# Kernel tuning notes

Hardware: AMD Instinct MI355X
Metric: run time of the kernel (lower is better)

The kernel has to match this reference:

```python
import jax, jax.numpy as jnp
import numpy as np

ALPHA = 0.5  # smooth_quant migration strength
N_TOKENS, D_MODEL = 32768, 1024  # square linear: d_in == d_out (required by diag_s @ weight)


def setup_inputs() -> dict:
    key = jax.random.key(0)
    k1, k2, k3 = jax.random.split(key, 3)
    x = jax.random.normal(k1, (N_TOKENS, D_MODEL), dtype=jnp.float32)
    weight = jax.random.normal(k2, (D_MODEL, D_MODEL), dtype=jnp.float32) * 0.02
    bias = jax.random.normal(k3, (D_MODEL,), dtype=jnp.float32) * 0.02
    return {"x": x, "weight": weight, "bias": bias}


def reference(x, weight, bias):
    # SmoothQuant rescale: per-in-channel maxima of activations and weight.
    max_act = jnp.max(x, axis=0) ** ALPHA                 # [D]
    max_w = jnp.max(weight, axis=0) ** (1.0 - ALPHA)      # [D] (max over out dim -> per in-channel)
    s = max_act / max_w                                   # [D] scale_fact
    # x_hat = x @ diag(s)^-1 ; expressed as the equivalent per-channel broadcast.
    x_hat = x / s                                         # [N, D]
    # weight_hat = diag(s) @ weight (square linear, row rescale).
    w_hat = s[:, None] * weight                           # [D, D]
    # nn.Linear forward: x_hat @ weight_hat^T + bias
    return x_hat @ w_hat.T + bias
```

## Files before the change

### kernel.cpp

```cpp
#include <hip/hip_runtime.h>
#include <hip/hip_bf16.h>
#include <stdint.h>

#define D_MODEL 1024

typedef __attribute__((ext_vector_type(4))) float  f32x4;
typedef __attribute__((ext_vector_type(8))) __bf16 bf16x8;
typedef __attribute__((ext_vector_type(8))) unsigned short u16x8;
typedef __attribute__((ext_vector_type(4))) unsigned short u16x4;


__device__ __forceinline__ unsigned order_map(float x) {
    unsigned u = __float_as_uint(x);
    return (u & 0x80000000u) ? ~u : (u | 0x80000000u);
}
__device__ __forceinline__ float order_unmap(unsigned m) {
    unsigned b = (m & 0x80000000u) ? (m & 0x7fffffffu) : ~m;
    return __uint_as_float(b);
}
__device__ __forceinline__ unsigned short f2bf(float f) {
    unsigned u = __float_as_uint(f);
    u += 0x7fffu + ((u >> 16) & 1u);
    return (unsigned short)(u >> 16);
}


__global__ void init_u32(unsigned* __restrict__ p, int n) {
    int i = blockIdx.x * blockDim.x + threadIdx.x;
    if (i < n) p[i] = 0u;
}

__global__ void colmax_kernel(const float* __restrict__ src, int rows_per_slab,
                              int cols, unsigned* __restrict__ out_u) {
    int k = blockIdx.x * blockDim.x + threadIdx.x;
    const float* p = src + (size_t)blockIdx.y * rows_per_slab * cols + k;
    float m = -__builtin_inff();
#pragma unroll 4
    for (int r = 0; r < rows_per_slab; ++r)
        m = fmaxf(m, p[(size_t)r * cols]);
    atomicMax(&out_u[k], order_map(m));
}

#define CC_ROWS 16
__global__ __launch_bounds__(256)
void colmax_convert(const float* __restrict__ x,
                    float* __restrict__ partial,
                    unsigned short* __restrict__ xb) {
    int c4 = threadIdx.x * 4;
    size_t base = (size_t)blockIdx.x * CC_ROWS * D_MODEL + c4;
    f32x4 m4 = {-__builtin_inff(), -__builtin_inff(), -__builtin_inff(), -__builtin_inff()};
#pragma unroll 8
    for (int r = 0; r < CC_ROWS; ++r) {
        f32x4 v = *reinterpret_cast<const f32x4*>(&x[base + (size_t)r * D_MODEL]);
        u16x4 o;
#pragma unroll
        for (int e = 0; e < 4; ++e) { m4[e] = fmaxf(m4[e], v[e]); o[e] = f2bf(v[e]); }
        *reinterpret_cast<u16x4*>(&xb[base + (size_t)r * D_MODEL]) = o;
    }
    *reinterpret_cast<f32x4*>(&partial[(size_t)blockIdx.x * D_MODEL + c4]) = m4;
}

__global__ void reduce_partial(const float* __restrict__ partial,
                               unsigned* __restrict__ ma_u) {
    int col  = blockIdx.x * 256 + threadIdx.x;
    int b0   = blockIdx.y * 64;
    float m = -__builtin_inff();
#pragma unroll 8
    for (int i = 0; i < 64; ++i)
        m = fmaxf(m, partial[(size_t)(b0 + i) * D_MODEL + col]);
    atomicMax(&ma_u[col], order_map(m));
}

__global__ void scale_kernel(const unsigned* __restrict__ ma_u,
                             const unsigned* __restrict__ mw_u,
                             float* __restrict__ s) {
    int k = blockIdx.x * blockDim.x + threadIdx.x;
    if (k < D_MODEL) {
        float ma = order_unmap(ma_u[k]);
        float mw = order_unmap(mw_u[k]);
        s[k] = sqrtf(ma) / sqrtf(mw);
    }
}

__global__ void build_w_kernel(const float* __restrict__ W, const float* __restrict__ s,
                               unsigned short* __restrict__ Wp) {
    int j  = blockIdx.x;
    int k4 = threadIdx.x * 4;
    float sj = s[j];
    f32x4 w  = *reinterpret_cast<const f32x4*>(&W[(size_t)j * D_MODEL + k4]);
    f32x4 sk = *reinterpret_cast<const f32x4*>(&s[k4]);
    u16x4 o;
#pragma unroll
    for (int i = 0; i < 4; ++i) o[i] = f2bf(sj * w[i] / sk[i]);
    *reinterpret_cast<u16x4*>(&Wp[(size_t)j * D_MODEL + k4]) = o;
}

#define GBM 256
#define GBN 256
#define GBK 64
#define GNT (D_MODEL / GBK)

__global__ __launch_bounds__(512, 2)
void gemm_8ph(const unsigned short* __restrict__ Xb,
              const unsigned short* __restrict__ Wp,
              const float* __restrict__ bias,
              float* __restrict__ out) {
    __shared__ __align__(16) unsigned short As[2][GBM][GBK];
    __shared__ __align__(16) unsigned short Bs[2][GBN][GBK];

    int flat = blockIdx.x;
    int swz  = (flat & 7) * (gridDim.x >> 3) + (flat >> 3);
    const int nRowBlk = 32768 / GBM;
    int row0 = (swz % nRowBlk) * GBM;
    int col0 = (swz / nRowBlk) * GBN;

    int tid  = threadIdx.x;
    int wave = tid >> 6;
    int lane = tid & 63;
    int wr   = wave >> 2;
    int wc   = wave & 3;
    int l16  = lane & 15;
    int lq   = lane >> 4;
    int srow  = lane >> 3;
    int skoff = ((lane & 7) ^ srow) << 3;

    f32x4 acc[2][2][4][2];
#pragma unroll
    for (int mq = 0; mq < 2; ++mq)
#pragma unroll
        for (int nq = 0; nq < 2; ++nq)
#pragma unroll
            for (int m = 0; m < 4; ++m)
#pragma unroll
                for (int n = 0; n < 2; ++n)
                    acc[mq][nq][m][n] = (f32x4){0.f, 0.f, 0.f, 0.f};

    auto stageA = [&](int t, int b) {
        int k0 = t * GBK;
#pragma unroll
        for (int i = 0; i < 4; ++i) {
            int rg = wave * 4 + i;
            const unsigned short* g = Xb + (size_t)(row0 + rg * 8 + srow) * D_MODEL + k0 + skoff;
            __builtin_amdgcn_global_load_lds(
                (const __attribute__((address_space(1))) void*)g,
                (__attribute__((address_space(3))) void*)&As[b][rg * 8][0], 16, 0, 0);
        }
    };
    auto stageB = [&](int t, int b) {
        int k0 = t * GBK;
#pragma unroll
        for (int i = 0; i < 4; ++i) {
            int rg = wave * 4 + i;
            const unsigned short* g = Wp + (size_t)(col0 + rg * 8 + srow) * D_MODEL + k0 + skoff;
            __builtin_amdgcn_global_load_lds(
                (const __attribute__((address_space(1))) void*)g,
                (__attribute__((address_space(3))) void*)&Bs[b][rg * 8][0], 16, 0, 0);
        }
    };

    stageA(0, 0); stageB(0, 0);
    asm volatile("s_waitcnt vmcnt(0)" ::: "memory");
    __builtin_amdgcn_s_barrier();

#pragma unroll 1
    for (int t = 0; t < GNT; ++t) {
        int cur = t & 1;
        const char* Ab = (const char*)&As[cur][0][0];
        const char* Bb = (const char*)&Bs[cur][0][0];
        bool pf = (t < GNT - 1);

        bf16x8 af[4][2], bf[2][2];

        auto lda = [&](int mq, int m, int kk) {
            int row  = wr * 128 + mq * 64 + m * 16 + l16;
            int slot = (kk * 4 + lq) ^ (row & 7);
            return *reinterpret_cast<const bf16x8*>(Ab + row * 128 + slot * 16);
        };
        auto ldb = [&](int nq, int n, int kk) {
            int row  = wc * 64 + nq * 32 + n * 16 + l16;
            int slot = (kk * 4 + lq) ^ (row & 7);
            return *reinterpret_cast<const bf16x8*>(Bb + row * 128 + slot * 16);
        };
        auto quad = [&](int mq, int nq) {
            __builtin_amdgcn_s_setprio(1);
#pragma unroll
            for (int m = 0; m < 4; ++m)
#pragma unroll
                for (int n = 0; n < 2; ++n)
#pragma unroll
                    for (int kk = 0; kk < 2; ++kk)
                        acc[mq][nq][m][n] = __builtin_amdgcn_mfma_f32_16x16x32_bf16(
                            af[m][kk], bf[n][kk], acc[mq][nq][m][n], 0, 0, 0);
            __builtin_amdgcn_s_setprio(0);
        };

#pragma unroll
        for (int m = 0; m < 4; ++m)
#pragma unroll
            for (int kk = 0; kk < 2; ++kk) af[m][kk] = lda(0, m, kk);
#pragma unroll
        for (int n = 0; n < 2; ++n)
#pragma unroll
            for (int kk = 0; kk < 2; ++kk) bf[n][kk] = ldb(0, n, kk);
        if (pf) stageA(t + 1, cur ^ 1);
        __builtin_amdgcn_s_barrier();
        quad(0, 0);
        __builtin_amdgcn_s_barrier();

#pragma unroll
        for (int n = 0; n < 2; ++n)
#pragma unroll
            for (int kk = 0; kk < 2; ++kk) bf[n][kk] = ldb(1, n, kk);
        if (pf) stageB(t + 1, cur ^ 1);
        __builtin_amdgcn_s_barrier();
        quad(0, 1);
        __builtin_amdgcn_s_barrier();

#pragma unroll
        for (int m = 0; m < 4; ++m)
#pragma unroll
            for (int kk = 0; kk < 2; ++kk) af[m][kk] = lda(1, m, kk);
        __builtin_amdgcn_s_barrier();
        quad(1, 1);
        __builtin_amdgcn_s_barrier();

#pragma unroll
        for (int n = 0; n < 2; ++n)
#pragma unroll
            for (int kk = 0; kk < 2; ++kk) bf[n][kk] = ldb(0, n, kk);
        __builtin_amdgcn_s_barrier();
        quad(1, 0);
        if (pf) {
            asm volatile("s_waitcnt vmcnt(0)" ::: "memory");
            __builtin_amdgcn_s_barrier();
        }
    }

    int crow = row0 + wr * 128;
    int ccol = col0 + wc * 64;
#pragma unroll
    for (int nq = 0; nq < 2; ++nq)
#pragma unroll
        for (int n = 0; n < 2; ++n) {
            int col = ccol + nq * 32 + n * 16 + l16;
            float b = bias[col];
#pragma unroll
            for (int mq = 0; mq < 2; ++mq)
#pragma unroll
                for (int m = 0; m < 4; ++m) {
                    int r = crow + mq * 64 + m * 16 + lq * 4;
#pragma unroll
                    for (int q = 0; q < 4; ++q)
                        out[(size_t)(r + q) * D_MODEL + col] = acc[mq][nq][m][n][q] + b;
                }
        }
}

__global__ __launch_bounds__(256)
void gemm_fallback(const float* __restrict__ X, const unsigned short* __restrict__ Wp,
                   const float* __restrict__ bias, float* __restrict__ out, int N) {
    __shared__ __align__(16) unsigned short As[128][64];
    __shared__ __align__(16) unsigned short Bs[128][64];

    int flat = blockIdx.x;
    int swz  = ((gridDim.x & 7) == 0)
             ? (flat & 7) * (gridDim.x >> 3) + (flat >> 3) : flat;
    const int nColBlk = D_MODEL / 128;
    int row0 = (swz / nColBlk) * 128;
    int col0 = (swz % nColBlk) * 128;

    int tid  = threadIdx.x;
    int wave = tid >> 6;
    int lane = tid & 63;
    int wr   = wave >> 1;
    int wc   = wave & 1;
    int l16  = lane & 15;
    int srow  = lane >> 3;
    int skoff = ((lane & 7) ^ srow) << 3;

    f32x4 acc[4][4];
#pragma unroll
    for (int m = 0; m < 4; ++m)
#pragma unroll
        for (int n = 0; n < 4; ++n)
            acc[m][n] = (f32x4){0.f, 0.f, 0.f, 0.f};

    for (int k0 = 0; k0 < D_MODEL; k0 += 64) {
        __syncthreads();
#pragma unroll
        for (int i = 0; i < 4; ++i) {
            int c   = i * 256 + tid;
            int r   = c >> 3;
            int seg = c & 7;
            const float* gp = X + (size_t)(row0 + r) * D_MODEL + k0 + seg * 8;
            f32x4 x0 = *reinterpret_cast<const f32x4*>(gp);
            f32x4 x1 = *reinterpret_cast<const f32x4*>(gp + 4);
            u16x8 v;
#pragma unroll
            for (int e = 0; e < 4; ++e) { v[e] = f2bf(x0[e]); v[e + 4] = f2bf(x1[e]); }
            int off = (seg * 16) ^ ((r & 7) << 4);
            *reinterpret_cast<u16x8*>((char*)&As[0][0] + r * 128 + off) = v;
        }
#pragma unroll
        for (int i = 0; i < 4; ++i) {
            int r0 = (wave * 4 + i) * 8;
            const unsigned short* g = Wp + (size_t)(col0 + r0 + srow) * D_MODEL + k0 + skoff;
            __builtin_amdgcn_global_load_lds(
                (const __attribute__((address_space(1))) void*)g,
                (__attribute__((address_space(3))) void*)&Bs[r0][0], 16, 0, 0);
        }
        __syncthreads();
#pragma unroll
        for (int kk = 0; kk < 2; ++kk) {
            bf16x8 af[4], bf_[4];
#pragma unroll
            for (int m = 0; m < 4; ++m) {
                int row = wr * 64 + m * 16 + l16;
                int o   = ((lane >> 4) * 16 + kk * 64) ^ ((row & 7) << 4);
                af[m] = *reinterpret_cast<const bf16x8*>((const char*)&As[0][0] + row * 128 + o);
            }
#pragma unroll
            for (int n = 0; n < 4; ++n) {
                int row = wc * 64 + n * 16 + l16;
                int o   = ((lane >> 4) * 16 + kk * 64) ^ ((row & 7) << 4);
                bf_[n] = *reinterpret_cast<const bf16x8*>((const char*)&Bs[0][0] + row * 128 + o);
            }
#pragma unroll
            for (int m = 0; m < 4; ++m)
#pragma unroll
                for (int n = 0; n < 4; ++n)
                    acc[m][n] = __builtin_amdgcn_mfma_f32_16x16x32_bf16(
                        af[m], bf_[n], acc[m][n], 0, 0, 0);
        }
    }

    int crow = row0 + wr * 64;
    int ccol = col0 + wc * 64;
#pragma unroll
    for (int n = 0; n < 4; ++n) {
        int col = ccol + n * 16 + l16;
        float b = bias[col];
#pragma unroll
        for (int m = 0; m < 4; ++m) {
            int r = crow + m * 16 + (lane >> 4) * 4;
#pragma unroll
            for (int q = 0; q < 4; ++q)
                out[(size_t)(r + q) * D_MODEL + col] = acc[m][n][q] + b;
        }
    }
}


extern "C" void kernel_launch(void* const* d_in, const int* in_sizes, int n_in,
                              void* d_out, int out_size, void* d_ws, size_t ws_size,
                              hipStream_t stream) {
    const float* x    = (const float*)d_in[0];
    const float* w    = (const float*)d_in[1];
    const float* bias = (const float*)d_in[2];
    float* out        = (float*)d_out;
    const int N       = in_sizes[0] / D_MODEL;

    char* ws               = (char*)d_ws;
    unsigned*       ma_u   = (unsigned*)(ws);
    unsigned*       mw_u   = (unsigned*)(ws + 4096);
    float*          s      = (float*)(ws + 8192);
    unsigned short* Wp     = (unsigned short*)(ws + 16384);
    unsigned short* Xb     = (unsigned short*)(ws + 16384 + (size_t)D_MODEL * D_MODEL * 2);
    const int nPart        = N / CC_ROWS;
    float*          part   = (float*)(ws + 16384 + (size_t)D_MODEL * D_MODEL * 2
                                               + (size_t)N * D_MODEL * 2);

    size_t need = 16384 + (size_t)D_MODEL * D_MODEL * 2 + (size_t)N * D_MODEL * 2
                + (size_t)nPart * D_MODEL * 4;
    bool preconv = ws_size >= need;

    init_u32<<<8, 256, 0, stream>>>((unsigned*)ws, 2048);

    if (preconv) {
        colmax_convert<<<nPart, 256, 0, stream>>>(x, part, Xb);
        reduce_partial<<<dim3(D_MODEL / 256, nPart / 64), 256, 0, stream>>>(part, ma_u);
    } else {
        colmax_kernel<<<dim3(D_MODEL / 256, 64), 256, 0, stream>>>(x, N / 64, D_MODEL, ma_u);
    }
    colmax_kernel<<<dim3(D_MODEL / 256, 16), 256, 0, stream>>>(w, D_MODEL / 16, D_MODEL, mw_u);
    scale_kernel<<<D_MODEL / 256, 256, 0, stream>>>(ma_u, mw_u, s);
    build_w_kernel<<<D_MODEL, 256, 0, stream>>>(w, s, Wp);

    if (preconv) {
        int nblk = (N / GBM) * (D_MODEL / GBN);
        gemm_8ph<<<nblk, 512, 0, stream>>>(Xb, Wp, bias, out);
    } else {
        int nblk = (N / 128) * (D_MODEL / 128);
        gemm_fallback<<<nblk, 256, 0, stream>>>(x, Wp, bias, out, N);
    }
}
```

Baseline: 170.8 us.

## Replace 8-phase barrier schedule with upfront prefetch and XCD-aware tile mapping

The main GEMM loop drops the four barrier-separated quadrant phases. It now issues the next tile's global-to-LDS loads at the top of each iteration, loads all B fragments once, and runs two half-tile MFMA blocks with a single barrier per k-step. Block-to-tile mapping changes so that each XCD gets a fixed column block and a contiguous range of row blocks, which is meant to improve L2 reuse of the weight tile. Fewer barriers should cut stalls, but holding more B fragments raises register pressure. Issuing all prefetch loads at once also changes how memory latency overlaps with compute.

```diff
diff --git a/kernel.cpp b/kernel.cpp
--- a/kernel.cpp
+++ b/kernel.cpp
@@ -101,18 +101,18 @@
 #define GNT (D_MODEL / GBK)
 
 __global__ __launch_bounds__(512, 2)
-void gemm_8ph(const unsigned short* __restrict__ Xb,
-              const unsigned short* __restrict__ Wp,
-              const float* __restrict__ bias,
-              float* __restrict__ out) {
+void gemm_main(const unsigned short* __restrict__ Xb,
+               const unsigned short* __restrict__ Wp,
+               const float* __restrict__ bias,
+               float* __restrict__ out) {
     __shared__ __align__(16) unsigned short As[2][GBM][GBK];
     __shared__ __align__(16) unsigned short Bs[2][GBN][GBK];
 
     int flat = blockIdx.x;
-    int swz  = (flat & 7) * (gridDim.x >> 3) + (flat >> 3);
-    const int nRowBlk = 32768 / GBM;
-    int row0 = (swz % nRowBlk) * GBM;
-    int col0 = (swz / nRowBlk) * GBN;
+    int xcd  = flat & 7;
+    int idx  = flat >> 3;
+    int col0 = (xcd & 3) * GBN;
+    int row0 = ((xcd >> 2) * 64 + idx) * GBM;
 
     int tid  = threadIdx.x;
     int wave = tid >> 6;
@@ -165,11 +165,11 @@
 #pragma unroll 1
     for (int t = 0; t < GNT; ++t) {
         int cur = t & 1;
+        bool pf = (t + 1 < GNT);
         const char* Ab = (const char*)&As[cur][0][0];
         const char* Bb = (const char*)&Bs[cur][0][0];
-        bool pf = (t < GNT - 1);
-
-        bf16x8 af[4][2], bf[2][2];
+
+        if (pf) { stageA(t + 1, cur ^ 1); stageB(t + 1, cur ^ 1); }
 
         auto lda = [&](int mq, int m, int kk) {
             int row  = wr * 128 + mq * 64 + m * 16 + l16;
@@ -181,55 +181,55 @@
             int slot = (kk * 4 + lq) ^ (row & 7);
             return *reinterpret_cast<const bf16x8*>(Bb + row * 128 + slot * 16);
         };
-        auto quad = [&](int mq, int nq) {
+
+        bf16x8 bf[2][2][2];
+#pragma unroll
+        for (int nq = 0; nq < 2; ++nq)
+#pragma unroll
+            for (int n = 0; n < 2; ++n)
+#pragma unroll
+                for (int kk = 0; kk < 2; ++kk)
+                    bf[nq][n][kk] = ldb(nq, n, kk);
+
+        {
+            bf16x8 af[4][2];
+#pragma unroll
+            for (int m = 0; m < 4; ++m)
+#pragma unroll
+                for (int kk = 0; kk < 2; ++kk) af[m][kk] = lda(0, m, kk);
             __builtin_amdgcn_s_setprio(1);
 #pragma unroll
             for (int m = 0; m < 4; ++m)
 #pragma unroll
-                for (int n = 0; n < 2; ++n)
-#pragma unroll
-                    for (int kk = 0; kk < 2; ++kk)
-                        acc[mq][nq][m][n] = __builtin_amdgcn_mfma_f32_16x16x32_bf16(
-                            af[m][kk], bf[n][kk], acc[mq][nq][m][n], 0, 0, 0);
+                for (int nq = 0; nq < 2; ++nq)
+#pragma unroll
+                    for (int n = 0; n < 2; ++n)
+#pragma unroll
+                        for (int kk = 0; kk < 2; ++kk)
+                            acc[0][nq][m][n] = __builtin_amdgcn_mfma_f32_16x16x32_bf16(
+                                af[m][kk], bf[nq][n][kk], acc[0][nq][m][n], 0, 0, 0);
             __builtin_amdgcn_s_setprio(0);
-        };
-
-#pragma unroll
-        for (int m = 0; m < 4; ++m)
-#pragma unroll
-            for (int kk = 0; kk < 2; ++kk) af[m][kk] = lda(0, m, kk);
-#pragma unroll
-        for (int n = 0; n < 2; ++n)
-#pragma unroll
-            for (int kk = 0; kk < 2; ++kk) bf[n][kk] = ldb(0, n, kk);
-        if (pf) stageA(t + 1, cur ^ 1);
-        __builtin_amdgcn_s_barrier();
-        quad(0, 0);
-        __builtin_amdgcn_s_barrier();
-
-#pragma unroll
-        for (int n = 0; n < 2; ++n)
-#pragma unroll
-            for (int kk = 0; kk < 2; ++kk) bf[n][kk] = ldb(1, n, kk);
-        if (pf) stageB(t + 1, cur ^ 1);
-        __builtin_amdgcn_s_barrier();
-        quad(0, 1);
-        __builtin_amdgcn_s_barrier();
-
-#pragma unroll
-        for (int m = 0; m < 4; ++m)
-#pragma unroll
-            for (int kk = 0; kk < 2; ++kk) af[m][kk] = lda(1, m, kk);
-        __builtin_amdgcn_s_barrier();
-        quad(1, 1);
-        __builtin_amdgcn_s_barrier();
-
-#pragma unroll
-        for (int n = 0; n < 2; ++n)
-#pragma unroll
-            for (int kk = 0; kk < 2; ++kk) bf[n][kk] = ldb(0, n, kk);
-        __builtin_amdgcn_s_barrier();
-        quad(1, 0);
+        }
+        {
+            bf16x8 af[4][2];
+#pragma unroll
+            for (int m = 0; m < 4; ++m)
+#pragma unroll
+                for (int kk = 0; kk < 2; ++kk) af[m][kk] = lda(1, m, kk);
+            __builtin_amdgcn_s_setprio(1);
+#pragma unroll
+            for (int m = 0; m < 4; ++m)
+#pragma unroll
+                for (int nq = 0; nq < 2; ++nq)
+#pragma unroll
+                    for (int n = 0; n < 2; ++n)
+#pragma unroll
+                        for (int kk = 0; kk < 2; ++kk)
+                            acc[1][nq][m][n] = __builtin_amdgcn_mfma_f32_16x16x32_bf16(
+                                af[m][kk], bf[nq][n][kk], acc[1][nq][m][n], 0, 0, 0);
+            __builtin_amdgcn_s_setprio(0);
+        }
+
         if (pf) {
             asm volatile("s_waitcnt vmcnt(0)" ::: "memory");
             __builtin_amdgcn_s_barrier();
@@ -388,7 +388,7 @@
 
     if (preconv) {
         int nblk = (N / GBM) * (D_MODEL / GBN);
-        gemm_8ph<<<nblk, 512, 0, stream>>>(Xb, Wp, bias, out);
+        gemm_main<<<nblk, 512, 0, stream>>>(Xb, Wp, bias, out);
     } else {
         int nblk = (N / 128) * (D_MODEL / 128);
         gemm_fallback<<<nblk, 256, 0, stream>>>(x, Wp, bias, out, N);
```

After: 168.0 us. About the same (-1.7%).

## Split GEMM tile prefetch into four chunks with partial vmcnt waits and XCD-aware mapping

Applied to the files above, without the earlier changes.

The next K-tile prefetch is split into four chunks, one issued in each compute phase. Each phase waits with a partial s_waitcnt vmcnt(4) instead of a full drain at the end of the iteration, so global-to-LDS loads overlap the MFMA work more evenly. The block-to-tile mapping now places consecutive row blocks and all four column blocks on the same XCD to improve L2 reuse. The launch-bounds occupancy hint of 2 is dropped. The partial-wait counting must exactly match the number of outstanding loads, or a phase could read an LDS chunk before it has fully landed.

```diff
diff --git a/kernel.cpp b/kernel.cpp
--- a/kernel.cpp
+++ b/kernel.cpp
@@ -100,19 +100,19 @@
 #define GBK 64
 #define GNT (D_MODEL / GBK)
 
-__global__ __launch_bounds__(512, 2)
-void gemm_8ph(const unsigned short* __restrict__ Xb,
-              const unsigned short* __restrict__ Wp,
-              const float* __restrict__ bias,
-              float* __restrict__ out) {
+__global__ __launch_bounds__(512)
+void gemm_main(const unsigned short* __restrict__ Xb,
+               const unsigned short* __restrict__ Wp,
+               const float* __restrict__ bias,
+               float* __restrict__ out) {
     __shared__ __align__(16) unsigned short As[2][GBM][GBK];
     __shared__ __align__(16) unsigned short Bs[2][GBN][GBK];
 
-    int flat = blockIdx.x;
-    int swz  = (flat & 7) * (gridDim.x >> 3) + (flat >> 3);
-    const int nRowBlk = 32768 / GBM;
-    int row0 = (swz % nRowBlk) * GBM;
-    int col0 = (swz / nRowBlk) * GBN;
+    int flat  = blockIdx.x;
+    int xcd   = flat & 7;
+    int j     = flat >> 3;
+    int col0  = (j & 3) * GBN;
+    int row0  = ((xcd << 4) + (j >> 2)) * GBM;
 
     int tid  = threadIdx.x;
     int wave = tid >> 6;
@@ -135,51 +135,53 @@
                 for (int n = 0; n < 2; ++n)
                     acc[mq][nq][m][n] = (f32x4){0.f, 0.f, 0.f, 0.f};
 
-    auto stageA = [&](int t, int b) {
-        int k0 = t * GBK;
-#pragma unroll
-        for (int i = 0; i < 4; ++i) {
-            int rg = wave * 4 + i;
-            const unsigned short* g = Xb + (size_t)(row0 + rg * 8 + srow) * D_MODEL + k0 + skoff;
+    auto stageA_chunk = [&](int q, int t, int b) {
+#pragma unroll
+        for (int r = 0; r < 2; ++r) {
+            int rb = q * 64 + r * 128 + wave * 8;
+            const unsigned short* g =
+                Xb + (size_t)(row0 + rb + srow) * D_MODEL + t * GBK + skoff;
             __builtin_amdgcn_global_load_lds(
                 (const __attribute__((address_space(1))) void*)g,
-                (__attribute__((address_space(3))) void*)&As[b][rg * 8][0], 16, 0, 0);
+                (__attribute__((address_space(3))) void*)&As[b][rb][0], 16, 0, 0);
         }
     };
-    auto stageB = [&](int t, int b) {
-        int k0 = t * GBK;
-#pragma unroll
-        for (int i = 0; i < 4; ++i) {
-            int rg = wave * 4 + i;
-            const unsigned short* g = Wp + (size_t)(col0 + rg * 8 + srow) * D_MODEL + k0 + skoff;
+    auto stageB_chunk = [&](int q, int t, int b) {
+#pragma unroll
+        for (int r = 0; r < 2; ++r) {
+            int cb = q * 32 + (2 * r + (wave >> 2)) * 64 + (wave & 3) * 8;
+            const unsigned short* g =
+                Wp + (size_t)(col0 + cb + srow) * D_MODEL + t * GBK + skoff;
             __builtin_amdgcn_global_load_lds(
                 (const __attribute__((address_space(1))) void*)g,
-                (__attribute__((address_space(3))) void*)&Bs[b][rg * 8][0], 16, 0, 0);
+                (__attribute__((address_space(3))) void*)&Bs[b][cb][0], 16, 0, 0);
         }
     };
 
-    stageA(0, 0); stageB(0, 0);
+    stageA_chunk(0, 0, 0); stageB_chunk(0, 0, 0);
+    stageB_chunk(1, 0, 0); stageA_chunk(1, 0, 0);
     asm volatile("s_waitcnt vmcnt(0)" ::: "memory");
     __builtin_amdgcn_s_barrier();
+
+    bf16x8 af[4][2], bf[2][2];
 
 #pragma unroll 1
     for (int t = 0; t < GNT; ++t) {
         int cur = t & 1;
+        int nb  = cur ^ 1;
+        bool pf = (t + 1 < GNT);
         const char* Ab = (const char*)&As[cur][0][0];
         const char* Bb = (const char*)&Bs[cur][0][0];
-        bool pf = (t < GNT - 1);
-
-        bf16x8 af[4][2], bf[2][2];
 
         auto lda = [&](int mq, int m, int kk) {
             int row  = wr * 128 + mq * 64 + m * 16 + l16;
-            int slot = (kk * 4 + lq) ^ (row & 7);
-            return *reinterpret_cast<const bf16x8*>(Ab + row * 128 + slot * 16);
+            int o    = ((lq << 4) + (kk << 6)) ^ ((row & 7) << 4);
+            return *reinterpret_cast<const bf16x8*>(Ab + row * 128 + o);
         };
         auto ldb = [&](int nq, int n, int kk) {
             int row  = wc * 64 + nq * 32 + n * 16 + l16;
-            int slot = (kk * 4 + lq) ^ (row & 7);
-            return *reinterpret_cast<const bf16x8*>(Bb + row * 128 + slot * 16);
+            int o    = ((lq << 4) + (kk << 6)) ^ ((row & 7) << 4);
+            return *reinterpret_cast<const bf16x8*>(Bb + row * 128 + o);
         };
         auto quad = [&](int mq, int nq) {
             __builtin_amdgcn_s_setprio(1);
@@ -202,7 +204,8 @@
         for (int n = 0; n < 2; ++n)
 #pragma unroll
             for (int kk = 0; kk < 2; ++kk) bf[n][kk] = ldb(0, n, kk);
-        if (pf) stageA(t + 1, cur ^ 1);
+        if (pf) stageA_chunk(0, t + 1, nb);
+        asm volatile("s_waitcnt vmcnt(4)" ::: "memory");
         __builtin_amdgcn_s_barrier();
         quad(0, 0);
         __builtin_amdgcn_s_barrier();
@@ -211,7 +214,8 @@
         for (int n = 0; n < 2; ++n)
 #pragma unroll
             for (int kk = 0; kk < 2; ++kk) bf[n][kk] = ldb(1, n, kk);
-        if (pf) stageB(t + 1, cur ^ 1);
+        if (pf) stageB_chunk(0, t + 1, nb);
+        asm volatile("s_waitcnt vmcnt(4)" ::: "memory");
         __builtin_amdgcn_s_barrier();
         quad(0, 1);
         __builtin_amdgcn_s_barrier();
@@ -220,6 +224,8 @@
         for (int m = 0; m < 4; ++m)
 #pragma unroll
             for (int kk = 0; kk < 2; ++kk) af[m][kk] = lda(1, m, kk);
+        if (pf) stageB_chunk(1, t + 1, nb);
+        asm volatile("s_waitcnt vmcnt(4)" ::: "memory");
         __builtin_amdgcn_s_barrier();
         quad(1, 1);
         __builtin_amdgcn_s_barrier();
@@ -228,12 +234,11 @@
         for (int n = 0; n < 2; ++n)
 #pragma unroll
             for (int kk = 0; kk < 2; ++kk) bf[n][kk] = ldb(0, n, kk);
+        if (pf) stageA_chunk(1, t + 1, nb);
+        asm volatile("s_waitcnt vmcnt(4)" ::: "memory");
         __builtin_amdgcn_s_barrier();
         quad(1, 0);
-        if (pf) {
-            asm volatile("s_waitcnt vmcnt(0)" ::: "memory");
-            __builtin_amdgcn_s_barrier();
-        }
+        __builtin_amdgcn_s_barrier();
     }
 
     int crow = row0 + wr * 128;
@@ -388,7 +393,7 @@
 
     if (preconv) {
         int nblk = (N / GBM) * (D_MODEL / GBN);
-        gemm_8ph<<<nblk, 512, 0, stream>>>(Xb, Wp, bias, out);
+        gemm_main<<<nblk, 512, 0, stream>>>(Xb, Wp, bias, out);
     } else {
         int nblk = (N / 128) * (D_MODEL / 128);
         gemm_fallback<<<nblk, 256, 0, stream>>>(x, Wp, bias, out, N);
```

Measured after the change: 154.5 us. -9.5%, faster.
